# Optimization experiments

Measured on AMD Instinct MI355X. Metric: run time of the kernel, lower is better.

## Reference

```python
import jax, jax.numpy as jnp
import numpy as np
from jax import lax

BETA = 0.9
THRESHOLD = 1.0
NUM_STEPS = 100
NUM_INPUTS = 2
NUM_HIDDEN = 256
NUM_OUTPUTS = 1
BATCH = 4096

# snntorch ATan surrogate spike (default alpha=2.0): fwd is Heaviside,
# bwd is 1 / (1 + (pi * x)^2).
@jax.custom_vjp
def spike_fn(x):
    return (x > 0).astype(x.dtype)

def _spike_fwd(x):
    return spike_fn(x), x

def _spike_bwd(x, g):
    return (g / (1.0 + (jnp.pi * x) ** 2),)

spike_fn.defvjp(_spike_fwd, _spike_bwd)


def setup_inputs() -> dict:
    key = jax.random.key(0)
    ks = jax.random.split(key, 7)
    s1 = 1.0 / np.sqrt(NUM_INPUTS)
    s2 = 1.0 / np.sqrt(NUM_HIDDEN)
    return {
        "x": jax.random.normal(ks[0], (BATCH, NUM_INPUTS), jnp.float32),
        "W1": jax.random.uniform(ks[1], (NUM_INPUTS, NUM_HIDDEN), jnp.float32, -s1, s1),
        "b1": jax.random.uniform(ks[2], (NUM_HIDDEN,), jnp.float32, -s1, s1),
        "W2": jax.random.uniform(ks[3], (NUM_HIDDEN, NUM_HIDDEN), jnp.float32, -s2, s2),
        "b2": jax.random.uniform(ks[4], (NUM_HIDDEN,), jnp.float32, -s2, s2),
        "W3": jax.random.uniform(ks[5], (NUM_HIDDEN, NUM_OUTPUTS), jnp.float32, -s2, s2),
        "b3": jax.random.uniform(ks[6], (NUM_OUTPUTS,), jnp.float32, -s2, s2),
    }


def _lif_step(mem, cur):
    # snntorch Leaky (reset_mechanism='subtract'):
    #   reset computed from previous mem, detached from the graph
    reset = lax.stop_gradient((mem > THRESHOLD).astype(mem.dtype))
    mem = BETA * mem + cur - reset * THRESHOLD
    spk = spike_fn(mem - THRESHOLD)
    return mem, spk


def reference(x, W1, b1, W2, b2, W3, b3):
    # cur1 is identical every timestep (x is constant) -> hoist out of loop
    cur1 = x @ W1 + b1  # [B, H]
    mem0 = jnp.zeros_like(cur1)

    def step(carry, _):
        mem1, mem2, _ = carry
        mem1, spk1 = _lif_step(mem1, cur1)
        cur2 = spk1 @ W2 + b2
        mem2, spk2 = _lif_step(mem2, cur2)
        return (mem1, mem2, spk2), None

    (mem1, mem2, spk2), _ = lax.scan(step, (mem0, mem0, mem0), None, length=NUM_STEPS)
    cur3 = spk2 @ W3 + b3  # [B, num_outputs] -- output from the final step
    return cur3
```

## Files before the change

### kernel.cpp

```cpp
#include <hip/hip_runtime.h>


#define NB     4096
#define NH     256
#define NSTEPS 100
#define RPB    8

__global__ __launch_bounds__(256) void snn_fused(
    const float* __restrict__ x,
    const float* __restrict__ W1,
    const float* __restrict__ b1,
    const float* __restrict__ W2,
    const float* __restrict__ b2,
    const float* __restrict__ W3,
    const float* __restrict__ b3,
    float* __restrict__ out)
{
    const int t    = threadIdx.x;
    const int wave = t >> 6, lane = t & 63;
    const int r0   = blockIdx.x * RPB;

    __shared__ float  spks[RPB * NH];
    __shared__ double red[RPB][4];

    const float  w1a = W1[t];
    const float  w1b = W1[NH + t];
    const float  b1t = b1[t];
    const float  b2t = b2[t];
    const double w3t = (double)W3[t];

    float cur1[RPB], mem1[RPB], mem2[RPB], spk2[RPB];
    #pragma unroll
    for (int r = 0; r < RPB; ++r) {
        const float x0 = x[(r0 + r) * 2 + 0];
        const float x1 = x[(r0 + r) * 2 + 1];
        cur1[r] = __fadd_rn(__fmaf_rn(x1, w1b, __fmul_rn(x0, w1a)), b1t);
        mem1[r] = 0.0f;
        mem2[r] = 0.0f;
        spk2[r] = 0.0f;
    }

    for (int step = 0; step < NSTEPS; ++step) {
        #pragma unroll
        for (int r = 0; r < RPB; ++r) {
            float m   = mem1[r];
            float rst = (m > 1.0f) ? 1.0f : 0.0f;
            m = __fsub_rn(__fadd_rn(__fmul_rn(0.9f, m), cur1[r]), rst);
            mem1[r] = m;
            spks[r * NH + t] = (m > 1.0f) ? 1.0f : 0.0f;
        }
        __syncthreads();

        float acc[RPB];
        #pragma unroll
        for (int r = 0; r < RPB; ++r) acc[r] = 0.0f;

        const float* wp = W2 + t;
        const float* sp = spks;
        #pragma unroll 1
        for (int kg = 0; kg < NH / 4; ++kg) {
            const float w0 = wp[0 * NH];
            const float w1 = wp[1 * NH];
            const float w2v = wp[2 * NH];
            const float w3v = wp[3 * NH];
            wp += 4 * NH;
            #pragma unroll
            for (int r = 0; r < RPB; ++r) {
                const float4 s = *(const float4*)(sp + r * NH);
                float a = acc[r];
                a = __fmaf_rn(s.x, w0,  a);
                a = __fmaf_rn(s.y, w1,  a);
                a = __fmaf_rn(s.z, w2v, a);
                a = __fmaf_rn(s.w, w3v, a);
                acc[r] = a;
            }
            sp += 4;
        }

        #pragma unroll
        for (int r = 0; r < RPB; ++r) {
            float c2  = __fadd_rn(acc[r], b2t);
            float m   = mem2[r];
            float rst = (m > 1.0f) ? 1.0f : 0.0f;
            m = __fsub_rn(__fadd_rn(__fmul_rn(0.9f, m), c2), rst);
            mem2[r] = m;
            spk2[r] = (m > 1.0f) ? 1.0f : 0.0f;
        }
        __syncthreads();
    }

    #pragma unroll
    for (int r = 0; r < RPB; ++r) {
        double v = (double)spk2[r] * w3t;
        #pragma unroll
        for (int off = 32; off > 0; off >>= 1)
            v += __shfl_down(v, off);
        if (lane == 0) red[r][wave] = v;
    }
    __syncthreads();
    if (t < RPB) {
        out[r0 + t] = (float)(red[t][0] + red[t][1] + red[t][2] + red[t][3]
                              + (double)b3[0]);
    }
}

extern "C" void kernel_launch(void* const* d_in, const int* in_sizes, int n_in,
                              void* d_out, int out_size, void* d_ws, size_t ws_size,
                              hipStream_t stream) {
    const float* x  = (const float*)d_in[0];
    const float* W1 = (const float*)d_in[1];
    const float* b1 = (const float*)d_in[2];
    const float* W2 = (const float*)d_in[3];
    const float* b2 = (const float*)d_in[4];
    const float* W3 = (const float*)d_in[5];
    const float* b3 = (const float*)d_in[6];
    float* out = (float*)d_out;

    dim3 grid(NB / RPB);
    dim3 block(256);
    hipLaunchKernelGGL(snn_fused, grid, block, 0, stream,
                       x, W1, b1, W2, b2, W3, b3, out);
}
```

Measured before the change: 1.349 ms.

## Remap matmul threads to 4 rows by 2 columns for register tiling

Changes the hidden-layer matmul's thread mapping. Each thread now computes 2 output columns (j and j+128) for 4 batch rows instead of 1 column for all 8 rows. This halves the shared-memory spike reads per thread and reuses each loaded spike vector across two weights, at the cost of doubling the per-thread global W2 loads. The inner loop is also unrolled by 4, and the final reduction is regrouped to match the new mapping.

```diff
diff --git a/kernel.cpp b/kernel.cpp
--- a/kernel.cpp
+++ b/kernel.cpp
@@ -17,28 +17,37 @@
     float* __restrict__ out)
 {
     const int t    = threadIdx.x;
-    const int wave = t >> 6, lane = t & 63;
+    const int lane = t & 63;
+    const int jj   = t & 127;
+    const int rr   = t >> 7;
     const int r0   = blockIdx.x * RPB;
 
     __shared__ float  spks[RPB * NH];
-    __shared__ double red[RPB][4];
+    __shared__ double red[2][4][2];
 
-    const float  w1a = W1[t];
-    const float  w1b = W1[NH + t];
-    const float  b1t = b1[t];
-    const float  b2t = b2[t];
-    const double w3t = (double)W3[t];
+    const float w1a = W1[t];
+    const float w1b = W1[NH + t];
+    const float b1t = b1[t];
+    const float  b2lo = b2[jj];
+    const float  b2hi = b2[jj + 128];
+    const double w3lo = (double)W3[jj];
+    const double w3hi = (double)W3[jj + 128];
 
-    float cur1[RPB], mem1[RPB], mem2[RPB], spk2[RPB];
+    float cur1[RPB], mem1[RPB];
     #pragma unroll
     for (int r = 0; r < RPB; ++r) {
         const float x0 = x[(r0 + r) * 2 + 0];
         const float x1 = x[(r0 + r) * 2 + 1];
         cur1[r] = __fadd_rn(__fmaf_rn(x1, w1b, __fmul_rn(x0, w1a)), b1t);
         mem1[r] = 0.0f;
-        mem2[r] = 0.0f;
-        spk2[r] = 0.0f;
     }
+    float mem2[4][2], spk2f[4][2];
+    #pragma unroll
+    for (int ri = 0; ri < 4; ++ri)
+        for (int c = 0; c < 2; ++c) { mem2[ri][c] = 0.0f; spk2f[ri][c] = 0.0f; }
+
+    const float* wp = W2 + jj;
+    const float* sp = spks + rr * 4 * NH;
 
     for (int step = 0; step < NSTEPS; ++step) {
         #pragma unroll
@@ -51,55 +60,58 @@
         }
         __syncthreads();
 
-        float acc[RPB];
+        float acc[4][2];
         #pragma unroll
-        for (int r = 0; r < RPB; ++r) acc[r] = 0.0f;
+        for (int ri = 0; ri < 4; ++ri) { acc[ri][0] = 0.0f; acc[ri][1] = 0.0f; }
 
-        const float* wp = W2 + t;
-        const float* sp = spks;
-        #pragma unroll 1
+        #pragma unroll 4
         for (int kg = 0; kg < NH / 4; ++kg) {
-            const float w0 = wp[0 * NH];
-            const float w1 = wp[1 * NH];
-            const float w2v = wp[2 * NH];
-            const float w3v = wp[3 * NH];
-            wp += 4 * NH;
+            const float* wk = wp + (kg * 4) * NH;
+            float wl[4], wh[4];
             #pragma unroll
-            for (int r = 0; r < RPB; ++r) {
-                const float4 s = *(const float4*)(sp + r * NH);
-                float a = acc[r];
-                a = __fmaf_rn(s.x, w0,  a);
-                a = __fmaf_rn(s.y, w1,  a);
-                a = __fmaf_rn(s.z, w2v, a);
-                a = __fmaf_rn(s.w, w3v, a);
-                acc[r] = a;
+            for (int q = 0; q < 4; ++q) {
+                wl[q] = wk[q * NH];
+                wh[q] = wk[q * NH + 128];
             }
-            sp += 4;
+            #pragma unroll
+            for (int ri = 0; ri < 4; ++ri) {
+                const float4 s = *(const float4*)(sp + ri * NH + kg * 4);
+                float a0 = acc[ri][0], a1 = acc[ri][1];
+                a0 = __fmaf_rn(s.x, wl[0], a0);  a1 = __fmaf_rn(s.x, wh[0], a1);
+                a0 = __fmaf_rn(s.y, wl[1], a0);  a1 = __fmaf_rn(s.y, wh[1], a1);
+                a0 = __fmaf_rn(s.z, wl[2], a0);  a1 = __fmaf_rn(s.z, wh[2], a1);
+                a0 = __fmaf_rn(s.w, wl[3], a0);  a1 = __fmaf_rn(s.w, wh[3], a1);
+                acc[ri][0] = a0;  acc[ri][1] = a1;
+            }
         }
 
         #pragma unroll
-        for (int r = 0; r < RPB; ++r) {
-            float c2  = __fadd_rn(acc[r], b2t);
-            float m   = mem2[r];
-            float rst = (m > 1.0f) ? 1.0f : 0.0f;
-            m = __fsub_rn(__fadd_rn(__fmul_rn(0.9f, m), c2), rst);
-            mem2[r] = m;
-            spk2[r] = (m > 1.0f) ? 1.0f : 0.0f;
+        for (int ri = 0; ri < 4; ++ri) {
+            #pragma unroll
+            for (int c = 0; c < 2; ++c) {
+                float c2  = __fadd_rn(acc[ri][c], (c == 0) ? b2lo : b2hi);
+                float m   = mem2[ri][c];
+                float rst = (m > 1.0f) ? 1.0f : 0.0f;
+                m = __fsub_rn(__fadd_rn(__fmul_rn(0.9f, m), c2), rst);
+                mem2[ri][c] = m;
+                spk2f[ri][c] = (m > 1.0f) ? 1.0f : 0.0f;
+            }
         }
         __syncthreads();
     }
 
+    const int wpair = (t >> 6) & 1;
     #pragma unroll
-    for (int r = 0; r < RPB; ++r) {
-        double v = (double)spk2[r] * w3t;
+    for (int ri = 0; ri < 4; ++ri) {
+        double v = (double)spk2f[ri][0] * w3lo + (double)spk2f[ri][1] * w3hi;
         #pragma unroll
         for (int off = 32; off > 0; off >>= 1)
             v += __shfl_down(v, off);
-        if (lane == 0) red[r][wave] = v;
+        if (lane == 0) red[rr][ri][wpair] = v;
     }
     __syncthreads();
     if (t < RPB) {
-        out[r0 + t] = (float)(red[t][0] + red[t][1] + red[t][2] + red[t][3]
+        out[r0 + t] = (float)(red[t >> 2][t & 3][0] + red[t >> 2][t & 3][1]
                               + (double)b3[0]);
     }
 }
```

Measured after the change: 1.137 ms. -15.7%, faster.
